# Performance work log

Hardware: AMD Instinct MI355X
Metric: run time of the kernel (lower is better)

Reference implementation:

```python
import jax, jax.numpy as jnp
import numpy as np

MS0 = 4            # base sector size (ms[0])
MS1 = 4            # top sector size (r=[1] -> ms[-1]=ms0)
Q = 2              # q_length (Ising spin states)
C = 512            # c_length
LAYERS = 2
B = 256
L = 16
FS = MS0 * MS0 - 1  # neighborhood size, excludes target pixel


def setup_inputs():
    key = jax.random.key(0)
    ks = jax.random.split(key, 8)
    v = jax.random.randint(ks[0], (B, L, L), 0, Q, dtype=jnp.int32)
    u = v.astype(jnp.float32)
    emb = jax.random.normal(ks[1], (FS, Q, C), dtype=jnp.float32)  # fs embedding tables

    def lin_w(k, out_d, in_d):
        b = 1.0 / np.sqrt(in_d)
        return jax.random.uniform(k, (out_d, in_d), minval=-b, maxval=b, dtype=jnp.float32)

    def lin_b(k, out_d, in_d):
        b = 1.0 / np.sqrt(in_d)
        return jax.random.uniform(k, (out_d,), minval=-b, maxval=b, dtype=jnp.float32)

    k2a, k2b = jax.random.split(ks[2])
    k3a, k3b = jax.random.split(ks[3])
    mlp_w1 = lin_w(k2a, C, C)
    mlp_b1 = lin_b(k2b, C, C)
    mlp_w2 = lin_w(k3a, Q, C)
    mlp_b2 = lin_b(k3b, Q, C)

    def lstm_p(k, in_d):
        k1, k2, k3, k4 = jax.random.split(k, 4)
        b = 1.0 / np.sqrt(C)
        wi = jax.random.uniform(k1, (4 * C, in_d), minval=-b, maxval=b, dtype=jnp.float32)
        wh = jax.random.uniform(k2, (4 * C, C), minval=-b, maxval=b, dtype=jnp.float32)
        bi = jax.random.uniform(k3, (4 * C,), minval=-b, maxval=b, dtype=jnp.float32)
        bh = jax.random.uniform(k4, (4 * C,), minval=-b, maxval=b, dtype=jnp.float32)
        return wi, wh, bi, bh

    w_ih0, w_hh0, b_ih0, b_hh0 = lstm_p(ks[4], MS1 * MS1)
    w_ih1, w_hh1, b_ih1, b_hh1 = lstm_p(ks[5], C)
    return dict(u=u, v=v, emb=emb,
                mlp_w1=mlp_w1, mlp_b1=mlp_b1, mlp_w2=mlp_w2, mlp_b2=mlp_b2,
                w_ih0=w_ih0, w_hh0=w_hh0, b_ih0=b_ih0, b_hh0=b_hh0,
                w_ih1=w_ih1, w_hh1=w_hh1, b_ih1=b_ih1, b_hh1=b_hh1)


def _forward(u, v, emb, mlp_w1, mlp_b1, mlp_w2, mlp_b2,
             w_ih0, w_hh0, b_ih0, b_hh0, w_ih1, w_hh1, b_ih1, b_hh1):
    n_sec = L // MS0
    margin = MS0 - 1
    lstm_params = ((w_ih0, w_hh0, b_ih0, b_hh0), (w_ih1, w_hh1, b_ih1, b_hh1))

    def lstm_step(x, state):
        # single-timestep multi-layer LSTM (eval mode, no dropout)
        h, c = state  # [LAYERS, B, C] each
        hs, cs = [], []
        inp = x
        for l, (wi, wh, bi, bh) in enumerate(lstm_params):
            g = inp @ wi.T + bi + h[l] @ wh.T + bh
            gi, gf, gg, go = jnp.split(g, 4, axis=-1)  # torch gate order i,f,g,o
            cn = jax.nn.sigmoid(gf) * c[l] + jax.nn.sigmoid(gi) * jnp.tanh(gg)
            hn = jax.nn.sigmoid(go) * jnp.tanh(cn)
            hs.append(hn)
            cs.append(cn)
            inp = hn
        return (jnp.stack(hs), jnp.stack(cs))

    zeros_state = lambda: (jnp.zeros((LAYERS, B, C), jnp.float32),
                           jnp.zeros((LAYERS, B, C), jnp.float32))
    memi = [zeros_state() for _ in range(n_sec)]
    memj = [zeros_state() for _ in range(n_sec)]
    sector = [0, 0]
    softout = jnp.zeros((B, L, L, Q), jnp.float32)
    nbr = jnp.arange(FS)[None, :]  # [1, FS] embedding-table indices
    key = jax.random.key(1234)

    for i in range(n_sec - 1):
        for j in range(n_sec - 1):
            si, sj = i * MS0, j * MS0
            ns0, ns1 = MS1 * (si // MS1), MS1 * (sj // MS1)
            if ns1 != sector[1]:
                sector = [ns0, ns1]
                for s in range(n_sec):
                    uv = u[:, s * MS1:(s + 1) * MS1, sector[1]:sector[1] + MS1].reshape(B, MS1 * MS1)
                    memj[s] = lstm_step(uv, memj[s])
            if ns0 != sector[0]:
                sector[0] = ns0
                uv = u[:, sector[0] - MS1:sector[0], sector[1]:sector[1] + MS1].reshape(B, MS1 * MS1)
                memi[sector[0] // MS1] = lstm_step(uv, memi[sector[0] // MS1])
            h0 = memj[i][0][0] + memi[j][0][0]  # layer-0 hidden sum, [B, C]
            for ii in range(MS0):
                for jj in range(MS0):
                    a, b = si + ii + 1, sj + jj + 1
                    pr, pc = a + margin, b + margin  # target pixel (bottom-right of patch)
                    patch = v[:, a:a + MS0, b:b + MS0].reshape(B, MS0 * MS0)[:, :FS]  # mask drops (margin,margin)
                    xemb = emb[nbr, patch, :].sum(axis=1)  # [B, C]
                    z = jax.nn.relu((xemb + h0) @ mlp_w1.T + mlp_b1)
                    logits = jax.nn.log_softmax(z @ mlp_w2.T + mlp_b2, axis=-1)  # [B, Q]
                    softout = softout.at[:, pr, pc].set(logits)
                    key, sub = jax.random.split(key)
                    samp = jax.random.categorical(sub, logits, axis=-1)  # [B]
                    v = v.at[:, pr, pc].set(samp.astype(v.dtype))
                    u = u.at[:, pr, pc].set(samp.astype(u.dtype))
    return softout, u, v


def reference(u, v, emb, mlp_w1, mlp_b1, mlp_w2, mlp_b2,
              w_ih0, w_hh0, b_ih0, b_hh0, w_ih1, w_hh1, b_ih1, b_hh1):
    return _forward(u, v, emb, mlp_w1, mlp_b1, mlp_w2, mlp_b2,
                    w_ih0, w_hh0, b_ih0, b_hh0, w_ih1, w_hh1, b_ih1, b_hh1)
```

## Files before the change

kernel.cpp:

```cpp
#include <hip/hip_runtime.h>
#include <cstdint>
#include <cstddef>

constexpr int NB = 256;
constexpr int NC = 512;
constexpr int NL = 16;
constexpr int NFS = 15;

#define PARTITIONABLE 1

struct TFOut { uint32_t a, b; };

__host__ __device__ constexpr uint32_t rotl32(uint32_t x, int d) {
  return (x << d) | (x >> (32 - d));
}

__host__ __device__ constexpr TFOut tf2x32(uint32_t k0, uint32_t k1,
                                           uint32_t x0, uint32_t x1) {
  uint32_t k2 = k0 ^ k1 ^ 0x1BD11BDAu;
  x0 += k0; x1 += k1;
  const int R0[4] = {13, 15, 26, 6};
  const int R1[4] = {17, 29, 16, 24};
  for (int i = 0; i < 4; i++) { x0 += x1; x1 = rotl32(x1, R0[i]); x1 ^= x0; }
  x0 += k1; x1 += k2 + 1u;
  for (int i = 0; i < 4; i++) { x0 += x1; x1 = rotl32(x1, R1[i]); x1 ^= x0; }
  x0 += k2; x1 += k0 + 2u;
  for (int i = 0; i < 4; i++) { x0 += x1; x1 = rotl32(x1, R0[i]); x1 ^= x0; }
  x0 += k0; x1 += k1 + 3u;
  for (int i = 0; i < 4; i++) { x0 += x1; x1 = rotl32(x1, R1[i]); x1 ^= x0; }
  x0 += k1; x1 += k2 + 4u;
  for (int i = 0; i < 4; i++) { x0 += x1; x1 = rotl32(x1, R0[i]); x1 ^= x0; }
  x0 += k2; x1 += k0 + 5u;
  return TFOut{x0, x1};
}

struct SubKeys { uint32_t v[288]; };

constexpr SubKeys make_subkeys() {
  SubKeys s{};
  uint32_t k0 = 0u, k1 = 1234u;
  for (int t = 0; t < 144; t++) {
#if PARTITIONABLE
    TFOut nk = tf2x32(k0, k1, 0u, 0u);
    TFOut sk = tf2x32(k0, k1, 0u, 1u);
    s.v[2 * t] = sk.a; s.v[2 * t + 1] = sk.b;
    k0 = nk.a; k1 = nk.b;
#else
    TFOut p0 = tf2x32(k0, k1, 0u, 2u);
    TFOut p1 = tf2x32(k0, k1, 1u, 3u);
    s.v[2 * t] = p0.b; s.v[2 * t + 1] = p1.b;
    k0 = p0.a; k1 = p1.a;
#endif
  }
  return s;
}

__constant__ SubKeys SUBKEYS = make_subkeys();

__device__ __forceinline__ float gumbel_from_bits(uint32_t bits) {
  uint32_t ub = (bits >> 9) | 0x3f800000u;
  float f = __uint_as_float(ub) - 1.0f;
  float u = (f == 0.0f) ? 1.17549435e-38f : f;
  float inner = logf(u);
  float outer = logf(-inner);
  return -outer;
}

typedef __attribute__((ext_vector_type(8))) short bf16x8;
typedef __attribute__((ext_vector_type(4))) float f32x4;

__device__ __forceinline__ void gl2lds16(const unsigned short* g,
                                         unsigned short* l) {
  __builtin_amdgcn_global_load_lds(
      (const __attribute__((address_space(1))) unsigned int*)g,
      (__attribute__((address_space(3))) unsigned int*)l, 16, 0, 0);
}

__device__ __forceinline__ uint32_t bf_rne(float x) {
  uint32_t u = __float_as_uint(x);
  return (u + 0x7fffu + ((u >> 16) & 1u)) >> 16;
}

__global__ __launch_bounds__(256) void setup_kernel(
    const float* __restrict__ u_in, const int* __restrict__ v_in,
    float* __restrict__ h0buf, float* __restrict__ cbuf,
    float* __restrict__ u_cur, int* __restrict__ v_cur,
    float* __restrict__ out_soft, float* __restrict__ out_u,
    float* __restrict__ out_v, unsigned int* __restrict__ az) {
  int idx = blockIdx.x * 256 + threadIdx.x;
  if (idx < 786432) h0buf[idx] = 0.0f;
  if (idx < 3 * NB * NC) cbuf[idx] = 0.0f;
  if (idx < 786432) az[idx] = 0u;
  if (idx < NB * NL * NL) {
    float uv = u_in[idx];
    int vv = v_in[idx];
    u_cur[idx] = uv;
    v_cur[idx] = vv;
    out_u[idx] = uv;
    out_v[idx] = (float)vv;
  }
  if (idx < NB * NL * NL * 2) out_soft[idx] = 0.0f;
}

__global__ __launch_bounds__(256) void split_w_kernel(
    const float* __restrict__ whh,
    unsigned short* __restrict__ Bhi, unsigned short* __restrict__ Blo) {
  int idx = blockIdx.x * 256 + threadIdx.x;
  float x = whh[idx];
  uint32_t hb = bf_rne(x);
  float lo = x - __uint_as_float(hb << 16);
  Bhi[idx] = (unsigned short)hb;
  Blo[idx] = (unsigned short)bf_rne(lo);
}

__global__ __launch_bounds__(256) void wd_kernel(
    const float* __restrict__ emb, const float* __restrict__ w1,
    const float* __restrict__ b1, float* __restrict__ WD,
    float* __restrict__ A0v) {
  __shared__ double dvec[NC];
  int n = blockIdx.x, tid = threadIdx.x;
  for (int k = tid; k < NC; k += 256) {
    if (n < NFS) {
      dvec[k] = (double)emb[(n * 2 + 1) * NC + k] - (double)emb[(n * 2) * NC + k];
    } else {
      double s = 0.0;
      for (int nn = 0; nn < NFS; nn++) s += (double)emb[(nn * 2) * NC + k];
      dvec[k] = s;
    }
  }
  __syncthreads();
  for (int c = tid; c < NC; c += 256) {
    double acc = 0.0;
    const float* wrow = w1 + (size_t)c * NC;
    for (int k = 0; k < NC; k++) acc += dvec[k] * (double)wrow[k];
    if (n < NFS) WD[n * NC + c] = (float)acc;
    else         A0v[c] = (float)(acc + (double)b1[c]);
  }
}

__global__ __launch_bounds__(256) void lstm_fused2_kernel(
    const unsigned short* __restrict__ Ah_r, const unsigned short* __restrict__ Al_r,
    unsigned short* __restrict__ Ah_w, unsigned short* __restrict__ Al_w,
    const unsigned short* __restrict__ Bhi, const unsigned short* __restrict__ Blo,
    const float* __restrict__ wih, const float* __restrict__ u_cur,
    const float* __restrict__ bih, const float* __restrict__ bhh,
    float* __restrict__ cbuf, float* __restrict__ h_out, int col0) {
  __shared__ __align__(16) unsigned short SM[24576];
  __shared__ float uvs[32][16];

  unsigned short* sA  = SM;
  unsigned short* sAl = SM + 4096;
  unsigned short* sB  = SM + 8192;
  unsigned short* sBl = SM + 16384;

  int bx = blockIdx.x;
  int rt = bx >> 5;
  int ct = bx & 31;
  int tid = threadIdx.x;
  int w = tid >> 6, lane = tid & 63;
  int l15 = lane & 15, kg = lane >> 4;
  int sw = (l15 >> 1) & 3;
  int grow0 = rt * 32;
  int s = rt >> 3;
  int b0 = (rt & 7) * 32;

  {
    int idx = tid;
    for (int t = 0; t < 2; t++, idx += 256) {
      int r = idx >> 4, nn = idx & 15;
      uvs[r][nn] =
          u_cur[(b0 + r) * 256 + (s * 4 + (nn >> 2)) * 16 + col0 + (nn & 3)];
    }
  }

  f32x4 acc[2][4];
#pragma unroll
  for (int i = 0; i < 2; i++)
#pragma unroll
    for (int j = 0; j < 4; j++) acc[i][j] = (f32x4){0.f, 0.f, 0.f, 0.f};

  for (int kc = 0; kc < 4; kc++) {
    int k0 = w * 128 + kc * 32;
    if (kc > 0) __syncthreads();
#pragma unroll
    for (int q = 0; q < 2; q++) {
      int slot = q * 64 + lane;
      int r = slot >> 2;
      int c2 = (slot & 3) ^ ((r >> 1) & 3);
      size_t so = (size_t)(grow0 + r) * 512 + k0 + c2 * 8;
      gl2lds16(Ah_r + so, sA + w * 1024 + q * 512);
      gl2lds16(Al_r + so, sAl + w * 1024 + q * 512);
    }
#pragma unroll
    for (int q = 0; q < 4; q++) {
      int slot = q * 64 + lane;
      int r = slot >> 2;
      int c2 = (slot & 3) ^ ((r >> 1) & 3);
      int nidx = (r >> 4) * 512 + ct * 16 + (r & 15);
      size_t so = (size_t)nidx * 512 + k0 + c2 * 8;
      gl2lds16(Bhi + so, sB + w * 2048 + q * 512);
      gl2lds16(Blo + so, sBl + w * 2048 + q * 512);
    }
    __syncthreads();

    bf16x8 ah[2], al[2];
#pragma unroll
    for (int i = 0; i < 2; i++) {
      int ro = w * 1024 + (i * 16 + l15) * 32 + ((kg ^ sw) * 8);
      ah[i] = *(const bf16x8*)&sA[ro];
      al[i] = *(const bf16x8*)&sAl[ro];
    }
#pragma unroll
    for (int j = 0; j < 4; j++) {
      int ro = w * 2048 + (j * 16 + l15) * 32 + ((kg ^ sw) * 8);
      bf16x8 bh = *(const bf16x8*)&sB[ro];
      bf16x8 bl = *(const bf16x8*)&sBl[ro];
#pragma unroll
      for (int i = 0; i < 2; i++) {
        acc[i][j] = __builtin_amdgcn_mfma_f32_16x16x32_bf16(ah[i], bh,
                                                            acc[i][j], 0, 0, 0);
        acc[i][j] = __builtin_amdgcn_mfma_f32_16x16x32_bf16(ah[i], bl,
                                                            acc[i][j], 0, 0, 0);
        acc[i][j] = __builtin_amdgcn_mfma_f32_16x16x32_bf16(al[i], bh,
                                                            acc[i][j], 0, 0, 0);
      }
    }
  }

  float* red = (float*)SM;
  __syncthreads();
#pragma unroll
  for (int i = 0; i < 2; i++)
#pragma unroll
    for (int g = 0; g < 4; g++)
#pragma unroll
      for (int rr = 0; rr < 4; rr++) {
        int row = i * 16 + kg * 4 + rr;
        red[((w * 4 + g) * 32 + row) * 17 + l15] = acc[i][g][rr];
      }
  __syncthreads();

  int rbase = tid >> 4, c = tid & 15;
  int cglob = ct * 16 + c;
  float bi_[4], bh_[4];
#pragma unroll
  for (int g = 0; g < 4; g++) {
    bi_[g] = bih[g * 512 + cglob];
    bh_[g] = bhh[g * 512 + cglob];
  }
#pragma unroll
  for (int rh = 0; rh < 2; rh++) {
    int row = rh * 16 + rbase;
    int grow = grow0 + row;
    float uvr[16];
#pragma unroll
    for (int nn = 0; nn < 16; nn++) uvr[nn] = uvs[row][nn];
    float gv[4];
#pragma unroll
    for (int g = 0; g < 4; g++) {
      float v = 0.0f;
#pragma unroll
      for (int ww = 0; ww < 4; ww++)
        v += red[((ww * 4 + g) * 32 + row) * 17 + c];
      const float* wr = wih + (size_t)(g * 512 + cglob) * 16;
#pragma unroll
      for (int nn = 0; nn < 16; nn++) v = fmaf(uvr[nn], wr[nn], v);
      gv[g] = v + bi_[g] + bh_[g];
    }
    size_t off = (size_t)grow * NC + cglob;
    float c_old = cbuf[off];
    float sig_i = 1.0f / (1.0f + expf(-gv[0]));
    float sig_f = 1.0f / (1.0f + expf(-gv[1]));
    float tg    = tanhf(gv[2]);
    float sig_o = 1.0f / (1.0f + expf(-gv[3]));
    float cn = sig_f * c_old + sig_i * tg;
    float hn = sig_o * tanhf(cn);
    cbuf[off] = cn;
    h_out[off] = hn;
    uint32_t hb = bf_rne(hn);
    float lo = hn - __uint_as_float(hb << 16);
    Ah_w[off] = (unsigned short)hb;
    Al_w[off] = (unsigned short)bf_rne(lo);
  }
}

__global__ __launch_bounds__(256) void w1h0_kernel(
    const float* __restrict__ h_in,
    const float* __restrict__ w1, float* __restrict__ Hpart) {
  int bx = blockIdx.x;
  int ks = bx >> 5;
  int bt = (bx >> 3) & 3;
  int ct = bx & 7;
  int tid = threadIdx.x, tn = tid & 15, tb = tid >> 4;

  __shared__ float hs[64][36];
  __shared__ float wt[64][36];
  float acc[4][4] = {};
  const float* hbase = h_in + (size_t)(bt * 64) * NC;

  for (int kc = 0; kc < 2; kc++) {
    int k0 = ks * 64 + kc * 32;
    __syncthreads();
    for (int t = 0; t < 2; t++) {
      int idx = tid + t * 256;
      int row = idx >> 3, kk4 = idx & 7;
      *(float4*)&hs[row][kk4 * 4] =
          *(const float4*)(hbase + (size_t)row * NC + k0 + kk4 * 4);
      int wrow = ct * 64 + row;
      *(float4*)&wt[row][kk4 * 4] =
          *(const float4*)(w1 + (size_t)wrow * NC + k0 + kk4 * 4);
    }
    __syncthreads();
#pragma unroll
    for (int kk4 = 0; kk4 < 8; kk4++) {
      float4 hv[4], wv[4];
#pragma unroll
      for (int i = 0; i < 4; i++) hv[i] = *(float4*)&hs[tb * 4 + i][kk4 * 4];
#pragma unroll
      for (int j = 0; j < 4; j++) wv[j] = *(float4*)&wt[tn + 16 * j][kk4 * 4];
#pragma unroll
      for (int i = 0; i < 4; i++)
#pragma unroll
        for (int j = 0; j < 4; j++)
          acc[i][j] += hv[i].x * wv[j].x + hv[i].y * wv[j].y +
                       hv[i].z * wv[j].z + hv[i].w * wv[j].w;
    }
  }
#pragma unroll
  for (int i = 0; i < 4; i++) {
    int b = bt * 64 + tb * 4 + i;
#pragma unroll
    for (int j = 0; j < 4; j++) {
      int cidx = ct * 64 + tn + 16 * j;
      Hpart[((size_t)ks * NB + b) * NC + cidx] = acc[i][j];
    }
  }
}

__global__ __launch_bounds__(64) void pixel_kernel(
    const float* __restrict__ WD, const float* __restrict__ A0v,
    const float* __restrict__ Hpart, const float* __restrict__ w2,
    const float* __restrict__ b2, float* __restrict__ u_cur,
    int* __restrict__ v_cur, float* __restrict__ out_soft,
    float* __restrict__ out_u, float* __restrict__ out_v,
    int si, int sj, int t_base) {
  int b = blockIdx.x, lane = threadIdx.x;
  __shared__ float gum[32];

  int widx = (lane < 49) ? lane : 48;
  int vv = v_cur[b * 256 + (si + 1 + widx / 7) * 16 + (sj + 1 + widx % 7)];
  unsigned long long mask = __ballot((lane < 49) && (vv != 0));

  if (lane < 32) {
    int t = t_base + (lane >> 1);
    uint32_t sk0 = SUBKEYS.v[2 * t], sk1 = SUBKEYS.v[2 * t + 1];
    uint32_t bits;
#if PARTITIONABLE
    TFOut o = tf2x32(sk0, sk1, 0u, (uint32_t)(2 * b + (lane & 1)));
    bits = o.a ^ o.b;
#else
    uint32_t f = (uint32_t)(2 * b + (lane & 1));
    if (f < 256u) { TFOut o = tf2x32(sk0, sk1, f, f + 256u); bits = o.a; }
    else          { TFOut o = tf2x32(sk0, sk1, f - 256u, f); bits = o.b; }
#endif
    gum[lane] = gumbel_from_bits(bits);
  }

  float wdreg[NFS][8];
#pragma unroll
  for (int n = 0; n < NFS; n++)
#pragma unroll
    for (int r = 0; r < 8; r++) wdreg[n][r] = WD[n * NC + lane + 64 * r];

  float w2r0[8], w2r1[8];
#pragma unroll
  for (int r = 0; r < 8; r++) {
    w2r0[r] = w2[lane + 64 * r];
    w2r1[r] = w2[NC + lane + 64 * r];
  }
  double b20 = (double)b2[0], b21 = (double)b2[1];

  float base[8];
#pragma unroll
  for (int r = 0; r < 8; r++) {
    int c = lane + 64 * r;
    float v = A0v[c];
#pragma unroll
    for (int ks = 0; ks < 8; ks++) v += Hpart[((size_t)ks * NB + b) * NC + c];
    base[r] = v;
  }
  __syncthreads();

#pragma unroll 1
  for (int ii = 0; ii < 4; ii++) {
#pragma unroll 1
    for (int jj = 0; jj < 4; jj++) {
      int bofs = ii * 7 + jj;
      float acc[8];
#pragma unroll
      for (int r = 0; r < 8; r++) acc[r] = base[r];
#pragma unroll
      for (int n = 0; n < NFS; n++) {
        const int OFF = (n / 4) * 7 + (n % 4);
        float pf = (float)((unsigned)((mask >> (bofs + OFF)) & 1ull));
#pragma unroll
        for (int r = 0; r < 8; r++) acc[r] = fmaf(pf, wdreg[n][r], acc[r]);
      }
      double d0 = 0.0, d1 = 0.0;
#pragma unroll
      for (int r = 0; r < 8; r++) {
        float z = fmaxf(acc[r], 0.0f);
        d0 += (double)z * (double)w2r0[r];
        d1 += (double)z * (double)w2r1[r];
      }
#pragma unroll
      for (int off = 32; off > 0; off >>= 1) {
        d0 += __shfl_xor(d0, off, 64);
        d1 += __shfl_xor(d1, off, 64);
      }
      float r0 = (float)(d0 + b20);
      float r1 = (float)(d1 + b21);
      float m = fmaxf(r0, r1);
      float s0 = r0 - m, s1 = r1 - m;
      float lse = logf(expf(s0) + expf(s1));
      float l0 = s0 - lse, l1 = s1 - lse;
      int pidx = ii * 4 + jj;
      float a0 = l0 + gum[2 * pidx];
      float a1 = l1 + gum[2 * pidx + 1];
      int samp = (a1 > a0) ? 1 : 0;
      int tbit = bofs + 24;
      mask = (mask & ~(1ull << tbit)) | ((unsigned long long)samp << tbit);
      if (lane == 0) {
        int pr = si + ii + 4, pc = sj + jj + 4;
        size_t so = ((size_t)(b * 16 + pr) * 16 + pc) * 2;
        out_soft[so] = l0;
        out_soft[so + 1] = l1;
        int po = b * 256 + pr * 16 + pc;
        float fs = (float)samp;
        u_cur[po] = fs;
        v_cur[po] = samp;
        out_u[po] = fs;
        out_v[po] = fs;
      }
    }
  }
}

extern "C" void kernel_launch(void* const* d_in, const int* in_sizes, int n_in,
                              void* d_out, int out_size, void* d_ws,
                              size_t ws_size, hipStream_t stream) {
  (void)in_sizes; (void)n_in; (void)out_size; (void)ws_size;
  const float* u_in = (const float*)d_in[0];
  const int*   v_in = (const int*)d_in[1];
  const float* emb  = (const float*)d_in[2];
  const float* w1   = (const float*)d_in[3];
  const float* b1   = (const float*)d_in[4];
  const float* w2   = (const float*)d_in[5];
  const float* b2   = (const float*)d_in[6];
  const float* wih  = (const float*)d_in[7];
  const float* whh  = (const float*)d_in[8];
  const float* bih  = (const float*)d_in[9];
  const float* bhh  = (const float*)d_in[10];

  float* ws = (float*)d_ws;
  const size_t HP = (size_t)3 * NB * NC;
  float* h0buf = ws;
  float* cbuf  = h0buf + 2 * HP;
  float* Hpart = cbuf + (size_t)3 * NB * NC;
  float* WDp   = Hpart + (size_t)8 * NB * NC;
  float* A0v   = WDp + NFS * NC;
  float* u_cur = A0v + NC;
  int*   v_cur = (int*)(u_cur + NB * NL * NL);
  unsigned short* Ahi = (unsigned short*)(v_cur + NB * NL * NL);
  unsigned short* Alo = Ahi + (size_t)2 * 768 * 512;
  unsigned short* Bhi = Alo + (size_t)2 * 768 * 512;
  unsigned short* Blo = Bhi + (size_t)2048 * 512;
  const size_t APAR = (size_t)768 * 512;

  float* out_soft = (float*)d_out;
  float* out_u = out_soft + NB * NL * NL * 2;
  float* out_v = out_u + NB * NL * NL;

  setup_kernel<<<dim3(4096), dim3(256), 0, stream>>>(
      u_in, v_in, h0buf, cbuf, u_cur, v_cur, out_soft, out_u, out_v,
      (unsigned int*)Ahi);
  split_w_kernel<<<dim3(4096), dim3(256), 0, stream>>>(whh, Bhi, Blo);
  wd_kernel<<<dim3(16), dim3(256), 0, stream>>>(emb, w1, b1, WDp, A0v);

  for (int k = 0; k < 9; k++) {
    if (k > 0) {
      int e = k - 1;
      int col0 = (e % 3 == 0) ? 4 : ((e % 3 == 1) ? 8 : 0);
      int rp = e & 1, wp = rp ^ 1;
      lstm_fused2_kernel<<<dim3(768), dim3(256), 0, stream>>>(
          Ahi + (size_t)rp * APAR, Alo + (size_t)rp * APAR,
          Ahi + (size_t)wp * APAR, Alo + (size_t)wp * APAR,
          Bhi, Blo, wih, u_cur, bih, bhh, cbuf,
          h0buf + (size_t)wp * HP, col0);
    }
    w1h0_kernel<<<dim3(256), dim3(256), 0, stream>>>(
        h0buf + (size_t)(k & 1) * HP + (size_t)(k / 3) * NB * NC, w1, Hpart);
    pixel_kernel<<<dim3(256), dim3(64), 0, stream>>>(
        WDp, A0v, Hpart, w2, b2, u_cur, v_cur, out_soft, out_u, out_v,
        (k / 3) * 4, (k % 3) * 4, k * 16);
  }
}
```

Before: 486.0 us.

## Retile LSTM GEMM to 96-row tiles with double-buffered full-K loop

Replaces the split-K LSTM recurrent GEMM (32-row tiles, each wave holding a K quarter, then a cross-wave LDS reduction) with 96-row tiles where each wave owns a 48x32 output sub-tile and loops over the full K in 16 steps. LDS staging is double-buffered so global-to-LDS loads for the next K chunk overlap MFMA work on the current one. The split-K reduction is dropped, and W_ih rows are loaded into registers once. The grid shrinks from 768 to 256 blocks, which may underfill the GPU's CUs and lengthen the serial K loop per block.

```diff
diff --git a/kernel.cpp b/kernel.cpp
--- a/kernel.cpp
+++ b/kernel.cpp
@@ -138,20 +138,15 @@
   }
 }
 
-__global__ __launch_bounds__(256) void lstm_fused2_kernel(
+__global__ __launch_bounds__(256) void lstm_fused3_kernel(
     const unsigned short* __restrict__ Ah_r, const unsigned short* __restrict__ Al_r,
     unsigned short* __restrict__ Ah_w, unsigned short* __restrict__ Al_w,
     const unsigned short* __restrict__ Bhi, const unsigned short* __restrict__ Blo,
     const float* __restrict__ wih, const float* __restrict__ u_cur,
     const float* __restrict__ bih, const float* __restrict__ bhh,
     float* __restrict__ cbuf, float* __restrict__ h_out, int col0) {
-  __shared__ __align__(16) unsigned short SM[24576];
-  __shared__ float uvs[32][16];
-
-  unsigned short* sA  = SM;
-  unsigned short* sAl = SM + 4096;
-  unsigned short* sB  = SM + 8192;
-  unsigned short* sBl = SM + 16384;
+  __shared__ __align__(16) unsigned short SM[2 * 10240];
+  __shared__ float uvs[96][16];
 
   int bx = blockIdx.x;
   int rt = bx >> 5;
@@ -159,98 +154,124 @@
   int tid = threadIdx.x;
   int w = tid >> 6, lane = tid & 63;
   int l15 = lane & 15, kg = lane >> 4;
-  int sw = (l15 >> 1) & 3;
-  int grow0 = rt * 32;
-  int s = rt >> 3;
-  int b0 = (rt & 7) * 32;
-
-  {
-    int idx = tid;
-    for (int t = 0; t < 2; t++, idx += 256) {
-      int r = idx >> 4, nn = idx & 15;
-      uvs[r][nn] =
-          u_cur[(b0 + r) * 256 + (s * 4 + (nn >> 2)) * 16 + col0 + (nn & 3)];
-    }
-  }
-
-  f32x4 acc[2][4];
-#pragma unroll
-  for (int i = 0; i < 2; i++)
-#pragma unroll
-    for (int j = 0; j < 4; j++) acc[i][j] = (f32x4){0.f, 0.f, 0.f, 0.f};
-
-  for (int kc = 0; kc < 4; kc++) {
-    int k0 = w * 128 + kc * 32;
-    if (kc > 0) __syncthreads();
-#pragma unroll
-    for (int q = 0; q < 2; q++) {
-      int slot = q * 64 + lane;
-      int r = slot >> 2;
-      int c2 = (slot & 3) ^ ((r >> 1) & 3);
-      size_t so = (size_t)(grow0 + r) * 512 + k0 + c2 * 8;
-      gl2lds16(Ah_r + so, sA + w * 1024 + q * 512);
-      gl2lds16(Al_r + so, sAl + w * 1024 + q * 512);
-    }
-#pragma unroll
-    for (int q = 0; q < 4; q++) {
-      int slot = q * 64 + lane;
-      int r = slot >> 2;
-      int c2 = (slot & 3) ^ ((r >> 1) & 3);
-      int nidx = (r >> 4) * 512 + ct * 16 + (r & 15);
-      size_t so = (size_t)nidx * 512 + k0 + c2 * 8;
-      gl2lds16(Bhi + so, sB + w * 2048 + q * 512);
-      gl2lds16(Blo + so, sBl + w * 2048 + q * 512);
-    }
+  int grow0 = rt * 96;
+  int wr0 = (w >> 1) * 48;
+  int wg0 = (w & 1) * 32;
+
+#pragma unroll
+  for (int q = 0; q < 6; q++) {
+    int idx = q * 256 + tid;
+    int r = idx >> 4, nn = idx & 15;
+    int grow = grow0 + r;
+    int s = grow >> 8, b = grow & 255;
+    uvs[r][nn] =
+        u_cur[b * 256 + (s * 4 + (nn >> 2)) * 16 + col0 + (nn & 3)];
+  }
+
+  auto STAGE = [&](int bufsel, int k0) {
+    unsigned short* base = SM + bufsel * 10240;
+#pragma unroll
+    for (int q = 0; q < 5; q++) {
+      int g = w + 4 * q;
+      int s = g * 64 + lane;
+      const unsigned short* src;
+      if (s < 768) {
+        int a = (s >= 384) ? 1 : 0;
+        int rs = s - a * 384;
+        int r = rs >> 2, kq = rs & 3;
+        int kqs = kq ^ ((r >> 1) & 3);
+        size_t so = (size_t)(grow0 + r) * 512 + k0 + kqs * 8;
+        src = (a ? Al_r : Ah_r) + so;
+      } else {
+        int a = (s >= 1024) ? 1 : 0;
+        int rs = s - 768 - a * 256;
+        int rr = rs >> 2, kq = rs & 3;
+        int kqs = kq ^ ((rr >> 1) & 3);
+        int n = (rr >> 4) * 512 + ct * 16 + (rr & 15);
+        size_t so = (size_t)n * 512 + k0 + kqs * 8;
+        src = (a ? Blo : Bhi) + so;
+      }
+      gl2lds16(src, base + (size_t)g * 512);
+    }
+  };
+
+  f32x4 acc[3][2];
+#pragma unroll
+  for (int i = 0; i < 3; i++)
+#pragma unroll
+    for (int j = 0; j < 2; j++) acc[i][j] = (f32x4){0.f, 0.f, 0.f, 0.f};
+
+  STAGE(0, 0);
+  __syncthreads();
+
+  for (int t = 0; t < 16; t++) {
+    int cur = t & 1;
+    if (t < 15) STAGE(cur ^ 1, (t + 1) * 32);
+    unsigned short* base = SM + cur * 10240;
+    bf16x8 ah[3], al[3], bh[2], bl[2];
+#pragma unroll
+    for (int i = 0; i < 3; i++) {
+      int r = wr0 + i * 16 + l15;
+      int off = r * 32 + (kg ^ ((r >> 1) & 3)) * 8;
+      ah[i] = *(const bf16x8*)&base[off];
+      al[i] = *(const bf16x8*)&base[3072 + off];
+    }
+#pragma unroll
+    for (int j = 0; j < 2; j++) {
+      int rr = wg0 + j * 16 + l15;
+      int off = rr * 32 + (kg ^ ((rr >> 1) & 3)) * 8;
+      bh[j] = *(const bf16x8*)&base[6144 + off];
+      bl[j] = *(const bf16x8*)&base[8192 + off];
+    }
+#pragma unroll
+    for (int i = 0; i < 3; i++)
+#pragma unroll
+      for (int j = 0; j < 2; j++) {
+        acc[i][j] = __builtin_amdgcn_mfma_f32_16x16x32_bf16(ah[i], bh[j],
+                                                            acc[i][j], 0, 0, 0);
+        acc[i][j] = __builtin_amdgcn_mfma_f32_16x16x32_bf16(ah[i], bl[j],
+                                                            acc[i][j], 0, 0, 0);
+        acc[i][j] = __builtin_amdgcn_mfma_f32_16x16x32_bf16(al[i], bh[j],
+                                                            acc[i][j], 0, 0, 0);
+      }
     __syncthreads();
-
-    bf16x8 ah[2], al[2];
-#pragma unroll
-    for (int i = 0; i < 2; i++) {
-      int ro = w * 1024 + (i * 16 + l15) * 32 + ((kg ^ sw) * 8);
-      ah[i] = *(const bf16x8*)&sA[ro];
-      al[i] = *(const bf16x8*)&sAl[ro];
-    }
-#pragma unroll
-    for (int j = 0; j < 4; j++) {
-      int ro = w * 2048 + (j * 16 + l15) * 32 + ((kg ^ sw) * 8);
-      bf16x8 bh = *(const bf16x8*)&sB[ro];
-      bf16x8 bl = *(const bf16x8*)&sBl[ro];
-#pragma unroll
-      for (int i = 0; i < 2; i++) {
-        acc[i][j] = __builtin_amdgcn_mfma_f32_16x16x32_bf16(ah[i], bh,
-                                                            acc[i][j], 0, 0, 0);
-        acc[i][j] = __builtin_amdgcn_mfma_f32_16x16x32_bf16(ah[i], bl,
-                                                            acc[i][j], 0, 0, 0);
-        acc[i][j] = __builtin_amdgcn_mfma_f32_16x16x32_bf16(al[i], bh,
-                                                            acc[i][j], 0, 0, 0);
-      }
-    }
-  }
-
-  float* red = (float*)SM;
-  __syncthreads();
-#pragma unroll
-  for (int i = 0; i < 2; i++)
-#pragma unroll
-    for (int g = 0; g < 4; g++)
-#pragma unroll
-      for (int rr = 0; rr < 4; rr++) {
-        int row = i * 16 + kg * 4 + rr;
-        red[((w * 4 + g) * 32 + row) * 17 + l15] = acc[i][g][rr];
-      }
-  __syncthreads();
-
-  int rbase = tid >> 4, c = tid & 15;
+  }
+
+  int c = tid & 15;
   int cglob = ct * 16 + c;
   float bi_[4], bh_[4];
+  float wihr[4][16];
 #pragma unroll
   for (int g = 0; g < 4; g++) {
     bi_[g] = bih[g * 512 + cglob];
     bh_[g] = bhh[g * 512 + cglob];
-  }
-#pragma unroll
-  for (int rh = 0; rh < 2; rh++) {
-    int row = rh * 16 + rbase;
+    const float4* wr = (const float4*)(wih + (size_t)(g * 512 + cglob) * 16);
+#pragma unroll
+    for (int f = 0; f < 4; f++) {
+      float4 v4 = wr[f];
+      wihr[g][f * 4 + 0] = v4.x;
+      wihr[g][f * 4 + 1] = v4.y;
+      wihr[g][f * 4 + 2] = v4.z;
+      wihr[g][f * 4 + 3] = v4.w;
+    }
+  }
+
+  float* ex = (float*)SM;
+#pragma unroll
+  for (int i = 0; i < 3; i++)
+#pragma unroll
+    for (int j = 0; j < 2; j++)
+#pragma unroll
+      for (int rr = 0; rr < 4; rr++) {
+        int row = wr0 + i * 16 + kg * 4 + rr;
+        int gcol = wg0 + j * 16 + l15;
+        ex[row * 68 + gcol] = acc[i][j][rr];
+      }
+  __syncthreads();
+
+#pragma unroll
+  for (int q = 0; q < 6; q++) {
+    int row = q * 16 + (tid >> 4);
     int grow = grow0 + row;
     float uvr[16];
 #pragma unroll
@@ -258,13 +279,9 @@
     float gv[4];
 #pragma unroll
     for (int g = 0; g < 4; g++) {
-      float v = 0.0f;
-#pragma unroll
-      for (int ww = 0; ww < 4; ww++)
-        v += red[((ww * 4 + g) * 32 + row) * 17 + c];
-      const float* wr = wih + (size_t)(g * 512 + cglob) * 16;
-#pragma unroll
-      for (int nn = 0; nn < 16; nn++) v = fmaf(uvr[nn], wr[nn], v);
+      float v = ex[row * 68 + g * 16 + c];
+#pragma unroll
+      for (int nn = 0; nn < 16; nn++) v = fmaf(uvr[nn], wihr[g][nn], v);
       gv[g] = v + bi_[g] + bh_[g];
     }
     size_t off = (size_t)grow * NC + cglob;
@@ -492,7 +509,7 @@
       int e = k - 1;
       int col0 = (e % 3 == 0) ? 4 : ((e % 3 == 1) ? 8 : 0);
       int rp = e & 1, wp = rp ^ 1;
-      lstm_fused2_kernel<<<dim3(768), dim3(256), 0, stream>>>(
+      lstm_fused3_kernel<<<dim3(256), dim3(256), 0, stream>>>(
           Ahi + (size_t)rp * APAR, Alo + (size_t)rp * APAR,
           Ahi + (size_t)wp * APAR, Alo + (size_t)wp * APAR,
           Bhi, Blo, wih, u_cur, bih, bhh, cbuf,
```

New measurement: 709.3 us. 1.46x slower.

## Assign LSTM tiles dynamically per XCD so blocks sharing weight columns hit the same L2

Applied to the files above, without the earlier changes.

Each LSTM block reads its hardware XCC id and takes a tile from a per-XCD atomic work queue. The queue first hands out tiles whose column groups belong to that XCD, so each XCD's L2 holds a fixed slice of the recurrent weights. When an XCD's own queue runs out, it falls back to stealing unclaimed tiles, with atomicExch on a taken flag keeping tiles unique. The cost is extra global atomics at block start, a separate zeroed queue region per step, and correctness that depends on the claim loop always finding a free tile.

```diff
diff --git a/kernel.cpp b/kernel.cpp
--- a/kernel.cpp
+++ b/kernel.cpp
@@ -86,11 +86,13 @@
     float* __restrict__ h0buf, float* __restrict__ cbuf,
     float* __restrict__ u_cur, int* __restrict__ v_cur,
     float* __restrict__ out_soft, float* __restrict__ out_u,
-    float* __restrict__ out_v, unsigned int* __restrict__ az) {
+    float* __restrict__ out_v, unsigned int* __restrict__ az,
+    int* __restrict__ qt) {
   int idx = blockIdx.x * 256 + threadIdx.x;
   if (idx < 786432) h0buf[idx] = 0.0f;
   if (idx < 3 * NB * NC) cbuf[idx] = 0.0f;
   if (idx < 786432) az[idx] = 0u;
+  if (idx < 8 * (8 + 768)) qt[idx] = 0;
   if (idx < NB * NL * NL) {
     float uv = u_in[idx];
     int vv = v_in[idx];
@@ -144,19 +146,43 @@
     const unsigned short* __restrict__ Bhi, const unsigned short* __restrict__ Blo,
     const float* __restrict__ wih, const float* __restrict__ u_cur,
     const float* __restrict__ bih, const float* __restrict__ bhh,
-    float* __restrict__ cbuf, float* __restrict__ h_out, int col0) {
+    float* __restrict__ cbuf, float* __restrict__ h_out, int col0,
+    int* __restrict__ qcnt, int* __restrict__ taken) {
   __shared__ __align__(16) unsigned short SM[24576];
   __shared__ float uvs[32][16];
+  __shared__ int tile_s;
 
   unsigned short* sA  = SM;
   unsigned short* sAl = SM + 4096;
   unsigned short* sB  = SM + 8192;
   unsigned short* sBl = SM + 16384;
 
-  int bx = blockIdx.x;
+  int tid = threadIdx.x;
+
+  if (tid == 0) {
+    uint32_t xc;
+    asm volatile("s_getreg_b32 %0, hwreg(HW_REG_XCC_ID)" : "=s"(xc));
+    xc &= 7u;
+    int T = -1;
+    while (T < 0) {
+      int idx = atomicAdd(&qcnt[xc], 1);
+      int cand;
+      if (idx < 96) {
+        int ctg = (int)xc * 4 + (idx & 3);
+        int rt_ = idx >> 2;
+        cand = rt_ * 32 + ctg;
+      } else {
+        cand = (idx - 96 + (int)xc * 96) % 768;
+      }
+      if (atomicExch(&taken[cand], 1) == 0) T = cand;
+    }
+    tile_s = T;
+  }
+  __syncthreads();
+  int bx = tile_s;
+  int ct = bx & 31;
   int rt = bx >> 5;
-  int ct = bx & 31;
-  int tid = threadIdx.x;
+
   int w = tid >> 6, lane = tid & 63;
   int l15 = lane & 15, kg = lane >> 4;
   int sw = (l15 >> 1) & 3;
@@ -475,6 +501,7 @@
   unsigned short* Alo = Ahi + (size_t)2 * 768 * 512;
   unsigned short* Bhi = Alo + (size_t)2 * 768 * 512;
   unsigned short* Blo = Bhi + (size_t)2048 * 512;
+  int* qt = (int*)(Blo + (size_t)2048 * 512);
   const size_t APAR = (size_t)768 * 512;
 
   float* out_soft = (float*)d_out;
@@ -483,7 +510,7 @@
 
   setup_kernel<<<dim3(4096), dim3(256), 0, stream>>>(
       u_in, v_in, h0buf, cbuf, u_cur, v_cur, out_soft, out_u, out_v,
-      (unsigned int*)Ahi);
+      (unsigned int*)Ahi, qt);
   split_w_kernel<<<dim3(4096), dim3(256), 0, stream>>>(whh, Bhi, Blo);
   wd_kernel<<<dim3(16), dim3(256), 0, stream>>>(emb, w1, b1, WDp, A0v);
 
@@ -492,11 +519,13 @@
       int e = k - 1;
       int col0 = (e % 3 == 0) ? 4 : ((e % 3 == 1) ? 8 : 0);
       int rp = e & 1, wp = rp ^ 1;
+      int* qcnt_e  = qt + (size_t)e * (8 + 768);
+      int* taken_e = qcnt_e + 8;
       lstm_fused2_kernel<<<dim3(768), dim3(256), 0, stream>>>(
           Ahi + (size_t)rp * APAR, Alo + (size_t)rp * APAR,
           Ahi + (size_t)wp * APAR, Alo + (size_t)wp * APAR,
           Bhi, Blo, wih, u_cur, bih, bhh, cbuf,
-          h0buf + (size_t)wp * HP, col0);
+          h0buf + (size_t)wp * HP, col0, qcnt_e, taken_e);
     }
     w1h0_kernel<<<dim3(256), dim3(256), 0, stream>>>(
         h0buf + (size_t)(k & 1) * HP + (size_t)(k / 3) * NB * NC, w1, Hpart);
```

Result: slower. 550.4 us (+13.3%).
